# Kernel tuning notes

Measured on AMD Instinct MI355X. Metric: run time of the kernel, lower is better.

The kernel has to match this reference:

```python
import jax, jax.numpy as jnp
import numpy as np


def _batch_conv2d(inputs, kernels):
    # inputs: [B, 1, H, W], kernels: [B, 1, 3, 3]; distinct kernel per sample
    # Implemented as a grouped conv: view inputs as [1, B, H, W], groups=B.
    B, _, H, W = inputs.shape
    out = jax.lax.conv_general_dilated(
        inputs.reshape(1, B, H, W),
        kernels,  # OIHW with O=B, I=1
        window_strides=(1, 1),
        padding=((1, 1), (1, 1)),
        feature_group_count=B,
        dimension_numbers=("NCHW", "OIHW", "NCHW"),
    )
    return out.reshape(B, 1, H, W)


def setup_inputs() -> dict:
    key = jax.random.key(0)
    k1, k2, k3 = jax.random.split(key, 3)
    B, m = 64, 512
    x = jax.random.normal(k1, (B, 1, m, m), dtype=jnp.float32)
    f = jax.random.normal(k2, (B, 1, m, m), dtype=jnp.float32)
    kernelA = jax.random.normal(k3, (B, 1, 3, 3), dtype=jnp.float32)
    return {"x": x, "f": f, "kernelA": kernelA}


def reference(x, f, kernelA):
    # One Jacobi-style smoothing step: x <- x + (f - A x) / 6
    Ax = _batch_conv2d(x, kernelA)
    x = x + (f - Ax) * (1.0 / 6.0)
    return x
```

## Files before the change

kernel.cpp:

```cpp
#include <hip/hip_runtime.h>

#define BB 64
#define HH 512
#define WW 512
#define NBLOCKS (BB * HH / 4)

struct Q { float4 v; float l, r; };

__device__ __forceinline__ void accumq(float4& q, const Q& w,
                                       float w0, float w1, float w2) {
    q.x += w0 * w.l   + w1 * w.v.x + w2 * w.v.y;
    q.y += w0 * w.v.x + w1 * w.v.y + w2 * w.v.z;
    q.z += w0 * w.v.y + w1 * w.v.z + w2 * w.v.w;
    q.w += w0 * w.v.z + w1 * w.v.w + w2 * w.r;
}

__global__ __launch_bounds__(256) void jacobi_v9_kernel(
    const float* __restrict__ x,
    const float* __restrict__ f,
    const float* __restrict__ k,
    float* __restrict__ out)
{
    const int tid  = threadIdx.x;
    const int lane = tid & 63;
    const int wv   = tid >> 6;

    const int b  = blockIdx.x >> 7;
    const int rg = blockIdx.x & 127;
    const int i  = (rg << 2) + wv;

    const int im = (i > 0)      ? i - 1 : 0;
    const int ip = (i < HH - 1) ? i + 1 : HH - 1;

    const size_t img = (size_t)b * (HH * WW);
    const float* xb = x + img;
    const float* fb = f + img;
    float*       ob = out + img;

    const float* kb = k + b * 9;
    const float k10 = kb[3], k11 = kb[4], k12 = kb[5];
    const float k00 = (i > 0)      ? kb[0] : 0.f;
    const float k01 = (i > 0)      ? kb[1] : 0.f;
    const float k02 = (i > 0)      ? kb[2] : 0.f;
    const float k20 = (i < HH - 1) ? kb[6] : 0.f;
    const float k21 = (i < HH - 1) ? kb[7] : 0.f;
    const float k22 = (i < HH - 1) ? kb[8] : 0.f;

    const int col = lane << 2;

    const float* pm = xb + (size_t)im * WW + col;
    const float* pc = xb + (size_t)i  * WW + col;
    const float* pp = xb + (size_t)ip * WW + col;
    const float* pf = fb + (size_t)i  * WW + col;
    float4 xma = *(const float4*)pm,  xmb = *(const float4*)(pm + 256);
    float4 xca = *(const float4*)pc,  xcb = *(const float4*)(pc + 256);
    float4 xpa = *(const float4*)pp,  xpb = *(const float4*)(pp + 256);
    float4 ffa = *(const float4*)pf,  ffb = *(const float4*)(pf + 256);
    __builtin_amdgcn_sched_barrier(0);

    float4 xa[3] = { xma, xca, xpa };
    float4 xq[3] = { xmb, xcb, xpb };
    Q A[3], B[3];
    #pragma unroll
    for (int t = 0; t < 3; ++t) {
        const float a_l  = __shfl_up(xa[t].w, 1);
        const float a_r  = __shfl_down(xa[t].x, 1);
        const float b_l  = __shfl_up(xq[t].w, 1);
        const float b_r  = __shfl_down(xq[t].x, 1);
        const float aw63 = __shfl(xa[t].w, 63);
        const float bx0  = __shfl(xq[t].x, 0);
        A[t].v = xa[t];
        B[t].v = xq[t];
        A[t].l = (lane == 0)  ? 0.f  : a_l;
        A[t].r = (lane == 63) ? bx0  : a_r;
        B[t].l = (lane == 0)  ? aw63 : b_l;
        B[t].r = (lane == 63) ? 0.f  : b_r;
    }

    float4 qa = make_float4(0.f, 0.f, 0.f, 0.f);
    float4 qb = make_float4(0.f, 0.f, 0.f, 0.f);
    accumq(qa, A[0], k00, k01, k02);
    accumq(qa, A[1], k10, k11, k12);
    accumq(qa, A[2], k20, k21, k22);
    accumq(qb, B[0], k00, k01, k02);
    accumq(qb, B[1], k10, k11, k12);
    accumq(qb, B[2], k20, k21, k22);

    const float inv6 = 1.f / 6.f;
    float4 oa, obq;
    oa.x  = xca.x + (ffa.x - qa.x) * inv6;
    oa.y  = xca.y + (ffa.y - qa.y) * inv6;
    oa.z  = xca.z + (ffa.z - qa.z) * inv6;
    oa.w  = xca.w + (ffa.w - qa.w) * inv6;
    obq.x = xcb.x + (ffb.x - qb.x) * inv6;
    obq.y = xcb.y + (ffb.y - qb.y) * inv6;
    obq.z = xcb.z + (ffb.z - qb.z) * inv6;
    obq.w = xcb.w + (ffb.w - qb.w) * inv6;

    float* po = ob + (size_t)i * WW + col;
    *(float4*)po         = oa;
    *(float4*)(po + 256) = obq;
}

extern "C" void kernel_launch(void* const* d_in, const int* in_sizes, int n_in,
                              void* d_out, int out_size, void* d_ws, size_t ws_size,
                              hipStream_t stream) {
    const float* x  = (const float*)d_in[0];
    const float* f  = (const float*)d_in[1];
    const float* kk = (const float*)d_in[2];
    float* out = (float*)d_out;

    jacobi_v9_kernel<<<NBLOCKS, 256, 0, stream>>>(x, f, kk, out);
}
```

Measured before the change: 165.6 us.

## Process four rows per wave with a rolling register window of halo rows

Each wave now computes four consecutive output rows instead of one, keeping the previous, current and next x rows (with shuffled horizontal halos) in registers and rotating them while prefetching the next x and f rows. This cuts redundant vertical halo reads of x from three rows per output row to about 1.5, and amortizes kernel indexing and weight loads. Block count drops fourfold and register pressure rises, reducing available parallelism and latency hiding; a launch-bounds occupancy hint is added.

```diff
diff --git a/kernel.cpp b/kernel.cpp
--- a/kernel.cpp
+++ b/kernel.cpp
@@ -3,7 +3,8 @@
 #define BB 64
 #define HH 512
 #define WW 512
-#define NBLOCKS (BB * HH / 4)
+#define LROWS 4
+#define NBLOCKS (BB * HH / LROWS / 4)
 
 struct Q { float4 v; float l, r; };
 
@@ -15,7 +16,23 @@
     q.w += w0 * w.v.z + w1 * w.v.w + w2 * w.r;
 }
 
-__global__ __launch_bounds__(256) void jacobi_v9_kernel(
+__device__ __forceinline__ void mkhalo(Q& A, Q& Bq, const float4 a,
+                                       const float4 bv, int lane) {
+    const float a_l  = __shfl_up(a.w, 1);
+    const float a_r  = __shfl_down(a.x, 1);
+    const float b_l  = __shfl_up(bv.w, 1);
+    const float b_r  = __shfl_down(bv.x, 1);
+    const float aw63 = __shfl(a.w, 63);
+    const float bx0  = __shfl(bv.x, 0);
+    A.v  = a;
+    Bq.v = bv;
+    A.l  = (lane == 0)  ? 0.f  : a_l;
+    A.r  = (lane == 63) ? bx0  : a_r;
+    Bq.l = (lane == 0)  ? aw63 : b_l;
+    Bq.r = (lane == 63) ? 0.f  : b_r;
+}
+
+__global__ __launch_bounds__(256, 6) void jacobi_v11_kernel(
     const float* __restrict__ x,
     const float* __restrict__ f,
     const float* __restrict__ k,
@@ -25,12 +42,9 @@
     const int lane = tid & 63;
     const int wv   = tid >> 6;
 
-    const int b  = blockIdx.x >> 7;
-    const int rg = blockIdx.x & 127;
-    const int i  = (rg << 2) + wv;
-
-    const int im = (i > 0)      ? i - 1 : 0;
-    const int ip = (i < HH - 1) ? i + 1 : HH - 1;
+    const int b  = blockIdx.x >> 5;
+    const int i0 = __builtin_amdgcn_readfirstlane(
+                       ((((blockIdx.x & 31) << 2) + wv) << 2));
 
     const size_t img = (size_t)b * (HH * WW);
     const float* xb = x + img;
@@ -38,68 +52,81 @@
     float*       ob = out + img;
 
     const float* kb = k + b * 9;
+    const float k00 = kb[0], k01 = kb[1], k02 = kb[2];
     const float k10 = kb[3], k11 = kb[4], k12 = kb[5];
-    const float k00 = (i > 0)      ? kb[0] : 0.f;
-    const float k01 = (i > 0)      ? kb[1] : 0.f;
-    const float k02 = (i > 0)      ? kb[2] : 0.f;
-    const float k20 = (i < HH - 1) ? kb[6] : 0.f;
-    const float k21 = (i < HH - 1) ? kb[7] : 0.f;
-    const float k22 = (i < HH - 1) ? kb[8] : 0.f;
+    const float k20 = kb[6], k21 = kb[7], k22 = kb[8];
 
     const int col = lane << 2;
 
-    const float* pm = xb + (size_t)im * WW + col;
-    const float* pc = xb + (size_t)i  * WW + col;
-    const float* pp = xb + (size_t)ip * WW + col;
-    const float* pf = fb + (size_t)i  * WW + col;
-    float4 xma = *(const float4*)pm,  xmb = *(const float4*)(pm + 256);
-    float4 xca = *(const float4*)pc,  xcb = *(const float4*)(pc + 256);
-    float4 xpa = *(const float4*)pp,  xpb = *(const float4*)(pp + 256);
-    float4 ffa = *(const float4*)pf,  ffb = *(const float4*)(pf + 256);
+    const int rm = (i0 > 0) ? i0 - 1 : 0;
+    const int rn = (i0 + 2 < HH) ? i0 + 2 : HH - 1;
+    const float* pm = xb + (size_t)rm * WW + col;
+    const float* pc = xb + (size_t)i0 * WW + col;
+    const float* pp = pc + WW;
+    const float* pn = xb + (size_t)rn * WW + col;
+    const float* pf = fb + (size_t)i0 * WW + col;
+    const float4 xma = *(const float4*)pm, xmb = *(const float4*)(pm + 256);
+    const float4 xca = *(const float4*)pc, xcb = *(const float4*)(pc + 256);
+    const float4 xpa = *(const float4*)pp, xpb = *(const float4*)(pp + 256);
+    float4 fca = *(const float4*)pf,       fcb = *(const float4*)(pf + 256);
+    float4 xna = *(const float4*)pn,       xnb = *(const float4*)(pn + 256);
+    float4 fna = *(const float4*)(pf + WW), fnb = *(const float4*)(pf + WW + 256);
     __builtin_amdgcn_sched_barrier(0);
 
-    float4 xa[3] = { xma, xca, xpa };
-    float4 xq[3] = { xmb, xcb, xpb };
-    Q A[3], B[3];
-    #pragma unroll
-    for (int t = 0; t < 3; ++t) {
-        const float a_l  = __shfl_up(xa[t].w, 1);
-        const float a_r  = __shfl_down(xa[t].x, 1);
-        const float b_l  = __shfl_up(xq[t].w, 1);
-        const float b_r  = __shfl_down(xq[t].x, 1);
-        const float aw63 = __shfl(xa[t].w, 63);
-        const float bx0  = __shfl(xq[t].x, 0);
-        A[t].v = xa[t];
-        B[t].v = xq[t];
-        A[t].l = (lane == 0)  ? 0.f  : a_l;
-        A[t].r = (lane == 63) ? bx0  : a_r;
-        B[t].l = (lane == 0)  ? aw63 : b_l;
-        B[t].r = (lane == 63) ? 0.f  : b_r;
-    }
-
-    float4 qa = make_float4(0.f, 0.f, 0.f, 0.f);
-    float4 qb = make_float4(0.f, 0.f, 0.f, 0.f);
-    accumq(qa, A[0], k00, k01, k02);
-    accumq(qa, A[1], k10, k11, k12);
-    accumq(qa, A[2], k20, k21, k22);
-    accumq(qb, B[0], k00, k01, k02);
-    accumq(qb, B[1], k10, k11, k12);
-    accumq(qb, B[2], k20, k21, k22);
+    Q Am, Bm, Ac, Bc, Ap, Bp;
+    mkhalo(Am, Bm, xma, xmb, lane);
+    mkhalo(Ac, Bc, xca, xcb, lane);
+    mkhalo(Ap, Bp, xpa, xpb, lane);
 
     const float inv6 = 1.f / 6.f;
-    float4 oa, obq;
-    oa.x  = xca.x + (ffa.x - qa.x) * inv6;
-    oa.y  = xca.y + (ffa.y - qa.y) * inv6;
-    oa.z  = xca.z + (ffa.z - qa.z) * inv6;
-    oa.w  = xca.w + (ffa.w - qa.w) * inv6;
-    obq.x = xcb.x + (ffb.x - qb.x) * inv6;
-    obq.y = xcb.y + (ffb.y - qb.y) * inv6;
-    obq.z = xcb.z + (ffb.z - qb.z) * inv6;
-    obq.w = xcb.w + (ffb.w - qb.w) * inv6;
+    #pragma unroll
+    for (int r = 0; r < LROWS; ++r) {
+        const int cur = i0 + r;
+        if (r > 0) {
+            Am = Ac; Bm = Bc;
+            Ac = Ap; Bc = Bp;
+            mkhalo(Ap, Bp, xna, xnb, lane);
+            fca = fna; fcb = fnb;
+            if (r < LROWS - 1) {
+                const int nx = (cur + 2 < HH) ? cur + 2 : HH - 1;
+                const float* px = xb + (size_t)nx * WW + col;
+                const float* pg = fb + (size_t)(cur + 1) * WW + col;
+                xna = *(const float4*)px; xnb = *(const float4*)(px + 256);
+                fna = *(const float4*)pg; fnb = *(const float4*)(pg + 256);
+            }
+            __builtin_amdgcn_sched_barrier(0);
+        }
 
-    float* po = ob + (size_t)i * WW + col;
-    *(float4*)po         = oa;
-    *(float4*)(po + 256) = obq;
+        const float w00 = (cur > 0)      ? k00 : 0.f;
+        const float w01 = (cur > 0)      ? k01 : 0.f;
+        const float w02 = (cur > 0)      ? k02 : 0.f;
+        const float w20 = (cur < HH - 1) ? k20 : 0.f;
+        const float w21 = (cur < HH - 1) ? k21 : 0.f;
+        const float w22 = (cur < HH - 1) ? k22 : 0.f;
+
+        float4 qa = make_float4(0.f, 0.f, 0.f, 0.f);
+        float4 qb = make_float4(0.f, 0.f, 0.f, 0.f);
+        accumq(qa, Am, w00, w01, w02);
+        accumq(qa, Ac, k10, k11, k12);
+        accumq(qa, Ap, w20, w21, w22);
+        accumq(qb, Bm, w00, w01, w02);
+        accumq(qb, Bc, k10, k11, k12);
+        accumq(qb, Bp, w20, w21, w22);
+
+        float4 oa, oq;
+        oa.x = Ac.v.x + (fca.x - qa.x) * inv6;
+        oa.y = Ac.v.y + (fca.y - qa.y) * inv6;
+        oa.z = Ac.v.z + (fca.z - qa.z) * inv6;
+        oa.w = Ac.v.w + (fca.w - qa.w) * inv6;
+        oq.x = Bc.v.x + (fcb.x - qb.x) * inv6;
+        oq.y = Bc.v.y + (fcb.y - qb.y) * inv6;
+        oq.z = Bc.v.z + (fcb.z - qb.z) * inv6;
+        oq.w = Bc.v.w + (fcb.w - qb.w) * inv6;
+
+        float* po = ob + (size_t)cur * WW + col;
+        *(float4*)po         = oa;
+        *(float4*)(po + 256) = oq;
+    }
 }
 
 extern "C" void kernel_launch(void* const* d_in, const int* in_sizes, int n_in,
@@ -110,5 +137,5 @@
     const float* kk = (const float*)d_in[2];
     float* out = (float*)d_out;
 
-    jacobi_v9_kernel<<<NBLOCKS, 256, 0, stream>>>(x, f, kk, out);
+    jacobi_v11_kernel<<<NBLOCKS, 256, 0, stream>>>(x, f, kk, out);
 }
```

After: 218.8 us. +32.2%, slower.
